# Performance work log

Measured on AMD Instinct MI355X. Metric: run time of the kernel, lower is better.

The kernel has to match this reference:

```python
import jax, jax.numpy as jnp
import numpy as np

ALPHA = 0.7
BETA = 0.3
GAMMA = 4.0
SMALL_LESION_WEIGHT = 10.0
SMOOTH = 1e-05
AREA_THRESH = 100  # region.area < 100 -> small lesion


def _label_components(mask):
    """8-connectivity connected-component labeling via min-label flooding.
    mask: [B,H,W] bool. Returns int32 labels in [0, H*W) for foreground,
    H*W (sentinel) for background. Equivalent partitioning to skimage.measure.label."""
    B, H, W = mask.shape
    BIG = H * W
    ids = jnp.arange(BIG, dtype=jnp.int32).reshape(1, H, W)
    lab0 = jnp.where(mask, ids, BIG)

    def neighbor_min(lab):
        p = jnp.pad(lab, ((0, 0), (1, 1), (1, 1)), constant_values=BIG)
        m = lab
        for di in range(3):  # 3x3 window = self + 8-neighbors
            for dj in range(3):
                m = jnp.minimum(m, p[:, di:di + H, dj:dj + W])
        return jnp.where(mask, m, BIG)

    def cond(state):
        return state[1]

    def body(state):
        lab, _ = state
        new = neighbor_min(lab)
        return new, jnp.any(new != lab)

    lab, _ = jax.lax.while_loop(cond, body, (lab0, jnp.array(True)))
    return lab


def _small_lesion_weights(targets):
    """targets: [B,1,H,W] float. Returns [B,1,H,W] weights: small_lesion_weight on
    pixels of connected components with area < AREA_THRESH, else 1.0."""
    t = targets[:, 0]                      # [B,H,W]
    mask = t > 0.5
    B, H, W = mask.shape
    BIG = H * W
    lab = _label_components(mask)          # [B,H,W] int32
    flat_lab = lab.reshape(B, BIG)
    ones = mask.astype(jnp.float32).reshape(B, BIG)
    # per-image component areas; background pixels fall into segment BIG
    areas = jax.vmap(lambda l, o: jax.ops.segment_sum(o, l, num_segments=BIG + 1))(flat_lab, ones)
    pix_area = jnp.take_along_axis(areas, flat_lab, axis=1).reshape(B, H, W)
    small = mask & (pix_area < AREA_THRESH)
    w = jnp.where(small, SMALL_LESION_WEIGHT, 1.0)
    return w[:, None, :, :]


def _bce_with_logits(x, t):
    # numerically stable elementwise BCE-with-logits
    return jnp.maximum(x, 0.0) - x * t + jnp.log1p(jnp.exp(-jnp.abs(x)))


def setup_inputs() -> dict:
    key = jax.random.key(0)
    k1, k2 = jax.random.split(key)
    B, C, H, W = 8, 1, 1024, 1024
    predictions = jax.random.normal(k1, (B, C, H, W), dtype=jnp.float32)
    targets = (jax.random.uniform(k2, (B, C, H, W)) < 0.05).astype(jnp.float32)
    return {"predictions": predictions, "targets": targets}


def reference(predictions, targets):
    p = jax.nn.sigmoid(predictions)

    # dice loss (global)
    inter = jnp.sum(p * targets)
    union = jnp.sum(p) + jnp.sum(targets)
    dice_loss = 1.0 - (2.0 * inter + SMOOTH) / (union + SMOOTH)

    # focal loss from logits
    bce = _bce_with_logits(predictions, targets)
    is_pos = targets == 1
    p_t = jnp.where(is_pos, p, 1.0 - p)
    alpha_t = jnp.where(is_pos, ALPHA, 1.0 - ALPHA)
    focal_loss = jnp.mean(alpha_t * (1.0 - p_t) ** GAMMA * bce)

    # tversky loss (FN-focused)
    TP = inter
    FP = jnp.sum((1.0 - targets) * p)
    FN = jnp.sum(targets * (1.0 - p))
    tversky_loss = 1.0 - (TP + SMOOTH) / (TP + ALPHA * FP + BETA * FN + SMOOTH)

    # small-lesion weighted BCE (weights are a non-diff function of targets)
    w = _small_lesion_weights(jax.lax.stop_gradient(targets))
    small_lesion_loss = jnp.mean(w * bce)

    return (dice_loss + focal_loss + tversky_loss + small_lesion_loss) / 4.0
```

## Files before the change

kernel.cpp:

```cpp
#include <hip/hip_runtime.h>

static constexpr int Bb = 8, Hh = 1024, Ww = 1024;
static constexpr int HW     = Hh * Ww;
static constexpr int NPIX   = Bb * HW;
static constexpr int NWORDS = NPIX / 64;
static constexpr int WPR    = Ww / 64;
static constexpr int WPI    = HW / 64;
static constexpr int NBK = 2048, NT = 256;
static constexpr int FNT = 1024;
static constexpr int FBG = 256;

typedef unsigned int u32;
typedef unsigned long long u64;

__device__ inline u32 lab_load(u32* L, u32 i) {
    return __hip_atomic_load(&L[i], __ATOMIC_RELAXED, __HIP_MEMORY_SCOPE_AGENT);
}
__device__ inline void lab_store(u32* L, u32 i, u32 v) {
    __hip_atomic_store(&L[i], v, __ATOMIC_RELAXED, __HIP_MEMORY_SCOPE_AGENT);
}
__device__ inline u32 find_root(u32* L, u32 x) {
    while (true) {
        u32 p = lab_load(L, x);
        if (p >= (u32)NPIX || p == x) return x;
        x = p;
    }
}
__device__ inline void union_labels(u32* L, u32 a, u32 b) {
    while (true) {
        a = find_root(L, a);
        b = find_root(L, b);
        if (a == b) return;
        if (a < b) { u32 t = a; a = b; b = t; }
        u32 old = atomicMin(&L[a], b);
        if (old == a || old >= (u32)NPIX) return;
        a = old;
    }
}

static constexpr u32 POISON = 0xAAAAAAAAu;
static constexpr u32 FLAGVAL = 0xC0FFEE00u;

__device__ inline double block_reduce(double v, double* lds) {
    for (int o = 32; o > 0; o >>= 1) v += __shfl_down(v, o, 64);
    int wave = threadIdx.x >> 6, lane = threadIdx.x & 63;
    __syncthreads();
    if (lane == 0) lds[wave] = v;
    __syncthreads();
    double r = 0.0;
    if (threadIdx.x == 0)
        for (int w = 0; w < (int)(blockDim.x >> 6); ++w) r += lds[w];
    return r;
}

__device__ inline float bce_pos(float x) {
    return fmaxf(-x, 0.0f) + __logf(1.0f + __expf(-fabsf(x)));
}

__device__ inline u64 spread4(u64 x) {
    x &= 0xFFFFull;
    x = (x | (x << 24)) & 0x000000FF000000FFull;
    x = (x | (x << 12)) & 0x000F000F000F000Full;
    x = (x | (x << 6))  & 0x0303030303030303ull;
    x = (x | (x << 3))  & 0x1111111111111111ull;
    return x;
}

__device__ inline void grid_barrier(u32* ctr, u32* flag) {
    __syncthreads();
    if (threadIdx.x == 0) {
        u32 old = __hip_atomic_fetch_add(ctr, 1u, __ATOMIC_RELAXED,
                                         __HIP_MEMORY_SCOPE_AGENT);
        if (old == POISON + (u32)FBG - 1u) {
            __hip_atomic_store(flag, FLAGVAL, __ATOMIC_RELAXED,
                               __HIP_MEMORY_SCOPE_AGENT);
        } else {
            while (__hip_atomic_load(flag, __ATOMIC_RELAXED,
                                     __HIP_MEMORY_SCOPE_AGENT) == POISON)
                __builtin_amdgcn_s_sleep(8);
        }
    }
    __syncthreads();
}

__global__ __launch_bounds__(NT) void k_init(const float4* __restrict__ pred4,
                                             const float4* __restrict__ targ4,
                                             u64* __restrict__ mask,
                                             double* __restrict__ part) {
    __shared__ double lds[NT / 64];
    float s_p = 0.f, s_t = 0.f, s_pt = 0.f, s_f = 0.f, s_b = 0.f, s_bf = 0.f;
    const int lane = threadIdx.x & 63;
    const int wid  = (blockIdx.x * NT + threadIdx.x) >> 6;

    float4 pv[4], tv[4];
    #pragma unroll
    for (int c = 0; c < 4; ++c) {
        const int chunk = (wid << 2) + c;
        pv[c] = pred4[chunk * 64 + lane];
        tv[c] = targ4[chunk * 64 + lane];
    }
    #pragma unroll
    for (int c = 0; c < 4; ++c) {
        const int chunk = (wid << 2) + c;
        const float* xa = &pv[c].x;
        const float* ta = &tv[c].x;
        u32 nib = 0;
        #pragma unroll
        for (int b = 0; b < 4; ++b) {
            const float x = xa[b], t = ta[b];
            const float ee  = __expf(-fabsf(x));
            const float rin = __builtin_amdgcn_rcpf(1.0f + ee);
            const float p   = (x >= 0.0f) ? rin : 1.0f - rin;
            const float bce = fmaxf(x, 0.0f) - x * t + __logf(1.0f + ee);
            const bool  pos = t > 0.5f;
            const float q1  = pos ? (1.0f - p) : p;
            const float at  = pos ? 0.7f : 0.3f;
            const float q2  = q1 * q1;
            s_p  += p;
            s_t  += t;
            s_pt += pos ? p : 0.0f;
            s_f  += at * q2 * q2 * bce;
            s_b  += bce;
            s_bf += pos ? bce : 0.0f;
            if (pos) nib |= 1u << b;
        }
        const u64 B0 = __ballot(nib & 1u);
        const u64 B1 = __ballot(nib & 2u);
        const u64 B2 = __ballot(nib & 4u);
        const u64 B3 = __ballot(nib & 8u);
        const int k = lane & 3;
        const u64 W = spread4(B0 >> (16 * k)) | (spread4(B1 >> (16 * k)) << 1)
                    | (spread4(B2 >> (16 * k)) << 2) | (spread4(B3 >> (16 * k)) << 3);
        if (lane < 4) mask[(chunk << 2) + lane] = W;
    }
    double r;
    r = block_reduce((double)s_p,  lds); if (threadIdx.x == 0) part[0 * NBK + blockIdx.x] = r;
    r = block_reduce((double)s_t,  lds); if (threadIdx.x == 0) part[1 * NBK + blockIdx.x] = r;
    r = block_reduce((double)s_pt, lds); if (threadIdx.x == 0) part[2 * NBK + blockIdx.x] = r;
    r = block_reduce((double)s_f,  lds); if (threadIdx.x == 0) part[3 * NBK + blockIdx.x] = r;
    r = block_reduce((double)s_b,  lds); if (threadIdx.x == 0) part[4 * NBK + blockIdx.x] = r;
    r = block_reduce((double)s_bf, lds); if (threadIdx.x == 0) part[5 * NBK + blockIdx.x] = r;
}

struct Nbr { u64 L, R, U, UL, UR, D, DL, DR; };
__device__ inline Nbr neighbors(const u64* __restrict__ mask, int wi, u64 cur) {
    int y  = (wi & (WPI - 1)) >> 4;
    int wx = wi & (WPR - 1);
    u64 lf = wx > 0       ? mask[wi - 1] : 0;
    u64 rt = wx < WPR - 1 ? mask[wi + 1] : 0;
    u64 up = 0, ul = 0, ur = 0, dn = 0, dl = 0, dr = 0;
    if (y > 0) {
        up = mask[wi - WPR];
        ul = wx > 0       ? mask[wi - WPR - 1] : 0;
        ur = wx < WPR - 1 ? mask[wi - WPR + 1] : 0;
    }
    if (y < Hh - 1) {
        dn = mask[wi + WPR];
        dl = wx > 0       ? mask[wi + WPR - 1] : 0;
        dr = wx < WPR - 1 ? mask[wi + WPR + 1] : 0;
    }
    Nbr n;
    n.L  = (cur << 1) | (lf >> 63);
    n.R  = (cur >> 1) | (rt << 63);
    n.U  = up;
    n.UL = (up << 1) | (ul >> 63);
    n.UR = (up >> 1) | (ur << 63);
    n.D  = dn;
    n.DL = (dn << 1) | (dl >> 63);
    n.DR = (dn >> 1) | (dr << 63);
    return n;
}

__device__ inline u64 half_mask(int t) {
    return (t & 1) ? 0xFFFFFFFF00000000ull : 0x00000000FFFFFFFFull;
}

static constexpr int B_CTR1 = 0, B_FLAG1 = 32, B_CTR2 = 64, B_FLAG2 = 96, B_DONE = 128;

__global__ __launch_bounds__(FNT, 4) void k_fused(const u64* __restrict__ mask,
                                                  u32* __restrict__ lab,
                                                  u32* __restrict__ area,
                                                  const float* __restrict__ pred,
                                                  double* __restrict__ part,
                                                  u32* __restrict__ bar,
                                                  float* __restrict__ out) {
    __shared__ double lds[FNT / 64];
    __shared__ int lastFlag;
    double* part_large = part + 6 * NBK;

    const int t  = blockIdx.x * FNT + threadIdx.x;
    const int wi = t >> 1;
    const u64 hm = half_mask(t);
    const u64 cur = mask[wi];
    const int base = wi << 6;

    u64 nonIso = 0, mrg = 0;
    u64 nL = 0, nU = 0, nUL = 0, nUR = 0;
    if (cur & hm) {
        Nbr n = neighbors(mask, wi, cur);
        nonIso = cur & (n.L | n.R | n.U | n.UL | n.UR | n.D | n.DL | n.DR) & hm;
        nL = n.L; nU = n.U; nUL = n.UL; nUR = n.UR;
        mrg = cur & (nL | nU | nUL | nUR) & hm;
    }

    u64 work = mrg;
    while (work) {
        int b = __builtin_ctzll(work); work &= work - 1;
        const u64 bit = 1ull << b;
        const u32 i = base + b;
        if (nL & bit) union_labels(lab, i, i - 1);
        if (nU & bit) union_labels(lab, i, i - Ww);
        else {
            if (nUL & bit) union_labels(lab, i, i - Ww - 1);
            if (nUR & bit) union_labels(lab, i, i - Ww + 1);
        }
    }
    grid_barrier(bar + B_CTR1, bar + B_FLAG1);

    u64 a = nonIso;
    while (a) {
        int b = __builtin_ctzll(a); a &= a - 1;
        const u32 i = base + b;
        const u32 r = find_root(lab, i);
        lab_store(lab, i, r);
        atomicAdd(&area[r], 1u);
    }
    grid_barrier(bar + B_CTR2, bar + B_FLAG2);

    float s = 0.f;
    u64 g = nonIso;
    while (g) {
        int b = __builtin_ctzll(g); g &= g - 1;
        const u32 i = base + b;
        const u32 r = lab_load(lab, i);
        const u32 cnt = __hip_atomic_load(&area[r], __ATOMIC_RELAXED,
                                          __HIP_MEMORY_SCOPE_AGENT) - POISON;
        if (cnt >= 100u)
            s += bce_pos(pred[i]);
    }
    double rr = block_reduce((double)s, lds);
    if (threadIdx.x == 0) {
        __hip_atomic_store(&part_large[blockIdx.x], rr, __ATOMIC_RELAXED,
                           __HIP_MEMORY_SCOPE_AGENT);
        asm volatile("s_waitcnt vmcnt(0)" ::: "memory");
        u32 old = __hip_atomic_fetch_add(bar + B_DONE, 1u, __ATOMIC_RELAXED,
                                         __HIP_MEMORY_SCOPE_AGENT);
        lastFlag = (old == POISON + (u32)FBG - 1u);
    }
    __syncthreads();
    if (!lastFlag) return;

    double sv[7] = {0, 0, 0, 0, 0, 0, 0};
    for (int j = threadIdx.x; j < NBK; j += FNT)
        #pragma unroll
        for (int k = 0; k < 6; ++k) sv[k] += part[k * NBK + j];
    for (int j = threadIdx.x; j < FBG; j += FNT)
        sv[6] += __hip_atomic_load(&part_large[j], __ATOMIC_RELAXED,
                                   __HIP_MEMORY_SCOPE_AGENT);
    double red[7];
    #pragma unroll
    for (int k = 0; k < 7; ++k) red[k] = block_reduce(sv[k], lds);
    if (threadIdx.x == 0) {
        double sum_p = red[0], sum_t = red[1], inter = red[2];
        double sum_f = red[3], sum_b = red[4], sum_bf = red[5], large_b = red[6];
        double small_b = sum_bf - large_b;
        double N = (double)NPIX;
        double dice    = 1.0 - (2.0 * inter + 1e-5) / (sum_p + sum_t + 1e-5);
        double focal   = sum_f / N;
        double FP = sum_p - inter, FN = sum_t - inter;
        double tversky = 1.0 - (inter + 1e-5) / (inter + 0.7 * FP + 0.3 * FN + 1e-5);
        double small   = (sum_b + 9.0 * small_b) / N;
        out[0] = (float)((dice + focal + tversky + small) * 0.25);
    }
}

extern "C" void kernel_launch(void* const* d_in, const int* in_sizes, int n_in,
                              void* d_out, int out_size, void* d_ws, size_t ws_size,
                              hipStream_t stream) {
    const float* pred = (const float*)d_in[0];
    const float* targ = (const float*)d_in[1];
    float* out = (float*)d_out;

    char* ws = (char*)d_ws;
    double* part = (double*)ws;
    u64* mask = (u64*)(ws + (size_t)(6 * NBK + FBG) * sizeof(double));
    u32* lab  = (u32*)(mask + NWORDS);
    u32* area = lab + NPIX;
    u32* bar  = area + NPIX;

    k_init <<<NBK, NT, 0, stream>>>((const float4*)pred, (const float4*)targ, mask, part);
    k_fused<<<FBG, FNT, 0, stream>>>(mask, lab, area, pred, part, bar, out);
}
```

Measured before the change: 151.3 us.

## Compact non-isolated foreground pixels into shared worklist for balanced union-find phases

Each block gathers its non-isolated foreground pixels, with packed neighbor flags, into a shared-memory worklist. The union, root-compression/area and weighted-BCE phases then iterate over that list with all threads striding through it, instead of each thread looping serially over its own bitmask. This targets warp divergence and load imbalance, since a few threads own many pixels while most own none. It costs 16KB of LDS per block, which may reduce occupancy with 1024-thread blocks, plus extra __syncthreads and an LDS atomic. An overflow path covers blocks with more than 4096 entries.

```diff
diff --git a/kernel.cpp b/kernel.cpp
--- a/kernel.cpp
+++ b/kernel.cpp
@@ -9,6 +9,7 @@
 static constexpr int NBK = 2048, NT = 256;
 static constexpr int FNT = 1024;
 static constexpr int FBG = 256;
+static constexpr int CAP = 4096;
 
 typedef unsigned int u32;
 typedef unsigned long long u64;
@@ -186,6 +187,8 @@
                                                   float* __restrict__ out) {
     __shared__ double lds[FNT / 64];
     __shared__ int lastFlag;
+    __shared__ u32 wl[CAP];
+    __shared__ u32 wl_n;
     double* part_large = part + 6 * NBK;
 
     const int t  = blockIdx.x * FNT + threadIdx.x;
@@ -194,49 +197,103 @@
     const u64 cur = mask[wi];
     const int base = wi << 6;
 
-    u64 nonIso = 0, mrg = 0;
+    if (threadIdx.x == 0) wl_n = 0;
+
+    u64 nonIso = 0;
     u64 nL = 0, nU = 0, nUL = 0, nUR = 0;
     if (cur & hm) {
         Nbr n = neighbors(mask, wi, cur);
         nonIso = cur & (n.L | n.R | n.U | n.UL | n.UR | n.D | n.DL | n.DR) & hm;
         nL = n.L; nU = n.U; nUL = n.UL; nUR = n.UR;
-        mrg = cur & (nL | nU | nUL | nUR) & hm;
-    }
-
-    u64 work = mrg;
-    while (work) {
-        int b = __builtin_ctzll(work); work &= work - 1;
-        const u64 bit = 1ull << b;
-        const u32 i = base + b;
-        if (nL & bit) union_labels(lab, i, i - 1);
-        if (nU & bit) union_labels(lab, i, i - Ww);
+    }
+    __syncthreads();
+
+    u64 ovf = 0;
+    {
+        int cnt = __builtin_popcountll(nonIso);
+        if (cnt) {
+            u32 slot = atomicAdd(&wl_n, (u32)cnt);
+            u64 w = nonIso;
+            while (w) {
+                int b = __builtin_ctzll(w); w &= w - 1;
+                if (slot < (u32)CAP) {
+                    const u32 f = (u32)((nL >> b) & 1) | ((u32)((nU >> b) & 1) << 1)
+                                | ((u32)((nUL >> b) & 1) << 2)
+                                | ((u32)((nUR >> b) & 1) << 3);
+                    wl[slot] = ((u32)(base + b) << 4) | f;
+                } else {
+                    ovf |= 1ull << b;
+                }
+                ++slot;
+            }
+        }
+    }
+    __syncthreads();
+    const u32 nwl = wl_n < (u32)CAP ? wl_n : (u32)CAP;
+
+    for (u32 e = threadIdx.x; e < nwl; e += FNT) {
+        const u32 ent = wl[e];
+        const u32 i = ent >> 4, f = ent & 15u;
+        if (f & 1u) union_labels(lab, i, i - 1);
+        if (f & 2u) union_labels(lab, i, i - Ww);
         else {
-            if (nUL & bit) union_labels(lab, i, i - Ww - 1);
-            if (nUR & bit) union_labels(lab, i, i - Ww + 1);
+            if (f & 4u) union_labels(lab, i, i - Ww - 1);
+            if (f & 8u) union_labels(lab, i, i - Ww + 1);
+        }
+    }
+    {
+        u64 w = ovf;
+        while (w) {
+            int b = __builtin_ctzll(w); w &= w - 1;
+            const u64 bit = 1ull << b;
+            const u32 i = base + b;
+            if (nL & bit) union_labels(lab, i, i - 1);
+            if (nU & bit) union_labels(lab, i, i - Ww);
+            else {
+                if (nUL & bit) union_labels(lab, i, i - Ww - 1);
+                if (nUR & bit) union_labels(lab, i, i - Ww + 1);
+            }
         }
     }
     grid_barrier(bar + B_CTR1, bar + B_FLAG1);
 
-    u64 a = nonIso;
-    while (a) {
-        int b = __builtin_ctzll(a); a &= a - 1;
-        const u32 i = base + b;
+    for (u32 e = threadIdx.x; e < nwl; e += FNT) {
+        const u32 i = wl[e] >> 4;
         const u32 r = find_root(lab, i);
         lab_store(lab, i, r);
         atomicAdd(&area[r], 1u);
     }
+    {
+        u64 w = ovf;
+        while (w) {
+            int b = __builtin_ctzll(w); w &= w - 1;
+            const u32 i = base + b;
+            const u32 r = find_root(lab, i);
+            lab_store(lab, i, r);
+            atomicAdd(&area[r], 1u);
+        }
+    }
     grid_barrier(bar + B_CTR2, bar + B_FLAG2);
 
     float s = 0.f;
-    u64 g = nonIso;
-    while (g) {
-        int b = __builtin_ctzll(g); g &= g - 1;
-        const u32 i = base + b;
+    for (u32 e = threadIdx.x; e < nwl; e += FNT) {
+        const u32 i = wl[e] >> 4;
         const u32 r = lab_load(lab, i);
         const u32 cnt = __hip_atomic_load(&area[r], __ATOMIC_RELAXED,
                                           __HIP_MEMORY_SCOPE_AGENT) - POISON;
         if (cnt >= 100u)
             s += bce_pos(pred[i]);
+    }
+    {
+        u64 w = ovf;
+        while (w) {
+            int b = __builtin_ctzll(w); w &= w - 1;
+            const u32 i = base + b;
+            const u32 r = lab_load(lab, i);
+            const u32 cnt = __hip_atomic_load(&area[r], __ATOMIC_RELAXED,
+                                              __HIP_MEMORY_SCOPE_AGENT) - POISON;
+            if (cnt >= 100u) s += bce_pos(pred[i]);
+        }
     }
     double rr = block_reduce((double)s, lds);
     if (threadIdx.x == 0) {
```

After: 140.4 us. -7.2%, faster.

## Do per-strip union-find in LDS and merge only strip-boundary components globally

Applied to the files above, without the earlier changes.

Each block now owns a 16-row strip and labels its components with union-find in shared memory. Per-root areas are packed into the LDS label word together with flag bits for a large component and for one that crosses the strip boundary. Only components touching a strip boundary go through global union-find and global area atomics, which cuts global atomic traffic and pointer chasing. The grid changes to 512 blocks of 512 threads with 64KB of dynamic LDS. The bit-packing adds complexity and limits each strip to 16K pixels and component sizes below 32K.

```diff
diff --git a/kernel.cpp b/kernel.cpp
--- a/kernel.cpp
+++ b/kernel.cpp
@@ -1,4 +1,7 @@
 #include <hip/hip_runtime.h>
+
+typedef unsigned int u32;
+typedef unsigned long long u64;
 
 static constexpr int Bb = 8, Hh = 1024, Ww = 1024;
 static constexpr int HW     = Hh * Ww;
@@ -7,11 +10,15 @@
 static constexpr int WPR    = Ww / 64;
 static constexpr int WPI    = HW / 64;
 static constexpr int NBK = 2048, NT = 256;
-static constexpr int FNT = 1024;
-static constexpr int FBG = 256;
-
-typedef unsigned int u32;
-typedef unsigned long long u64;
+static constexpr int FNT = 512, FBG = 512;
+static constexpr int SWORDS = NWORDS / FBG;
+static constexpr int SPX    = SWORDS * 64;
+
+static constexpr u32 POISON  = 0xAAAAAAAAu;
+static constexpr u32 FLAGVAL = 0xC0FFEE00u;
+static constexpr u32 LBITS = 0x3FFFu;
+static constexpr u32 BIGF  = 1u << 29;
+static constexpr u32 CROSSF = 1u << 30;
 
 __device__ inline u32 lab_load(u32* L, u32 i) {
     return __hip_atomic_load(&L[i], __ATOMIC_RELAXED, __HIP_MEMORY_SCOPE_AGENT);
@@ -38,8 +45,26 @@
     }
 }
 
-static constexpr u32 POISON = 0xAAAAAAAAu;
-static constexpr u32 FLAGVAL = 0xC0FFEE00u;
+__device__ inline u32 lds_load(u32* L, u32 x) {
+    return __hip_atomic_load(&L[x], __ATOMIC_RELAXED, __HIP_MEMORY_SCOPE_WORKGROUP);
+}
+__device__ inline void lds_store(u32* L, u32 x, u32 v) {
+    __hip_atomic_store(&L[x], v, __ATOMIC_RELAXED, __HIP_MEMORY_SCOPE_WORKGROUP);
+}
+__device__ inline u32 lfind(u32* L, u32 x) {
+    while (true) { u32 p = lds_load(L, x); if (p == x) return x; x = p; }
+}
+__device__ inline void lunion(u32* L, u32 a, u32 b) {
+    while (true) {
+        a = lfind(L, a);
+        b = lfind(L, b);
+        if (a == b) return;
+        if (a < b) { u32 t = a; a = b; b = t; }
+        u32 old = atomicMin(&L[a], b);
+        if (old == a) return;
+        a = old;
+    }
+}
 
 __device__ inline double block_reduce(double v, double* lds) {
     for (int o = 32; o > 0; o >>= 1) v += __shfl_down(v, o, 64);
@@ -184,83 +209,197 @@
                                                   double* __restrict__ part,
                                                   u32* __restrict__ bar,
                                                   float* __restrict__ out) {
-    __shared__ double lds[FNT / 64];
-    __shared__ int lastFlag;
+    extern __shared__ u32 llab[];
     double* part_large = part + 6 * NBK;
 
-    const int t  = blockIdx.x * FNT + threadIdx.x;
-    const int wi = t >> 1;
-    const u64 hm = half_mask(t);
-    const u64 cur = mask[wi];
-    const int base = wi << 6;
-
-    u64 nonIso = 0, mrg = 0;
-    u64 nL = 0, nU = 0, nUL = 0, nUR = 0;
+    const int tid  = threadIdx.x;
+    const int sbw  = blockIdx.x * SWORDS;
+    const int spx  = blockIdx.x * SPX;
+    const int lwi  = tid >> 1;
+    const int wi   = sbw + lwi;
+    const u64 hm   = half_mask(tid);
+    const u64 cur  = mask[wi];
+    const int lbase = lwi << 6;
+    const int y    = (wi & (WPI - 1)) >> 4;
+    const int ris  = y & 15;
+
+    u64 nL = 0, nU = 0, nUL = 0, nUR = 0, nUany = 0, nDany = 0;
     if (cur & hm) {
         Nbr n = neighbors(mask, wi, cur);
-        nonIso = cur & (n.L | n.R | n.U | n.UL | n.UR | n.D | n.DL | n.DR) & hm;
         nL = n.L; nU = n.U; nUL = n.UL; nUR = n.UR;
-        mrg = cur & (nL | nU | nUL | nUR) & hm;
-    }
-
-    u64 work = mrg;
-    while (work) {
-        int b = __builtin_ctzll(work); work &= work - 1;
-        const u64 bit = 1ull << b;
-        const u32 i = base + b;
-        if (nL & bit) union_labels(lab, i, i - 1);
-        if (nU & bit) union_labels(lab, i, i - Ww);
-        else {
-            if (nUL & bit) union_labels(lab, i, i - Ww - 1);
-            if (nUR & bit) union_labels(lab, i, i - Ww + 1);
+        nUany = n.U | n.UL | n.UR;
+        nDany = n.D | n.DL | n.DR;
+    }
+
+    for (u32 j = tid; j < (u32)SPX; j += FNT) llab[j] = j;
+    __syncthreads();
+
+    {
+        const u64 uU  = ris > 0 ? nU  : 0;
+        const u64 uUL = ris > 0 ? nUL : 0;
+        const u64 uUR = ris > 0 ? nUR : 0;
+        u64 w = cur & (nL | uU | uUL | uUR) & hm;
+        while (w) {
+            int b = __builtin_ctzll(w); w &= w - 1;
+            const u64 bit = 1ull << b;
+            const u32 li = lbase + b;
+            if (nL & bit) lunion(llab, li, li - 1);
+            if (uU & bit) lunion(llab, li, li - 1024);
+            else {
+                if (uUL & bit) lunion(llab, li, li - 1025);
+                if (uUR & bit) lunion(llab, li, li - 1023);
+            }
+        }
+    }
+    __syncthreads();
+
+    {
+        u64 w = cur & hm;
+        while (w) {
+            int b = __builtin_ctzll(w); w &= w - 1;
+            const u32 li = lbase + b;
+            const u32 r = lfind(llab, li);
+            if (r != li) lds_store(llab, li, r);
+        }
+    }
+    __syncthreads();
+
+    {
+        u64 w = cur & hm;
+        while (w) {
+            int b = __builtin_ctzll(w); w &= w - 1;
+            const u32 li = lbase + b;
+            const u32 r = lds_load(llab, li) & LBITS;
+            atomicAdd(&llab[r], 1u << 14);
+        }
+    }
+    __syncthreads();
+
+    if (cur & hm) {
+        if (ris == 0) {
+            u64 w = cur & nUany & hm;
+            while (w) {
+                int b = __builtin_ctzll(w); w &= w - 1;
+                const u32 r = lds_load(llab, lbase + b) & LBITS;
+                atomicOr(&llab[r], CROSSF);
+            }
+        }
+        if (ris == 15) {
+            u64 w = cur & nDany & hm;
+            while (w) {
+                int b = __builtin_ctzll(w); w &= w - 1;
+                const u32 r = lds_load(llab, lbase + b) & LBITS;
+                atomicOr(&llab[r], CROSSF);
+            }
+        }
+    }
+    __syncthreads();
+
+    {
+        u64 w = cur & hm;
+        while (w) {
+            int b = __builtin_ctzll(w); w &= w - 1;
+            const u32 li = lbase + b;
+            const u32 e = lds_load(llab, li);
+            if ((e & LBITS) == li && !(e & CROSSF)) {
+                const u32 cnt = (e >> 14) & 0x7FFFu;
+                if (cnt >= 100u) lds_store(llab, li, e | BIGF);
+            }
+        }
+    }
+    if (ris == 0 && (cur & hm)) {
+        u64 w = cur & nUany & hm;
+        while (w) {
+            int b = __builtin_ctzll(w); w &= w - 1;
+            const u64 bit = 1ull << b;
+            const u32 li = lbase + b;
+            const u32 gi = spx + li;
+            const u32 gr = spx + (lds_load(llab, li) & LBITS);
+            if (nU  & bit) union_labels(lab, gr, gi - Ww);
+            if (nUL & bit) union_labels(lab, gr, gi - Ww - 1);
+            if (nUR & bit) union_labels(lab, gr, gi - Ww + 1);
+        }
+    }
+    if (ris == 15 && (cur & hm)) {
+        u64 w = cur & nDany & hm;
+        while (w) {
+            int b = __builtin_ctzll(w); w &= w - 1;
+            const u32 li = lbase + b;
+            union_labels(lab, spx + li, spx + (lds_load(llab, li) & LBITS));
         }
     }
     grid_barrier(bar + B_CTR1, bar + B_FLAG1);
 
-    u64 a = nonIso;
-    while (a) {
-        int b = __builtin_ctzll(a); a &= a - 1;
-        const u32 i = base + b;
-        const u32 r = find_root(lab, i);
-        lab_store(lab, i, r);
-        atomicAdd(&area[r], 1u);
+    {
+        u64 w = cur & hm;
+        while (w) {
+            int b = __builtin_ctzll(w); w &= w - 1;
+            const u32 li = lbase + b;
+            const u32 e = lds_load(llab, li);
+            if ((e & LBITS) == li && (e & CROSSF)) {
+                const u32 gr = find_root(lab, spx + li);
+                lab_store(lab, spx + li, gr);
+                atomicAdd(&area[gr], (e >> 14) & 0x7FFFu);
+            }
+        }
     }
     grid_barrier(bar + B_CTR2, bar + B_FLAG2);
 
+    {
+        u64 w = cur & hm;
+        while (w) {
+            int b = __builtin_ctzll(w); w &= w - 1;
+            const u32 li = lbase + b;
+            const u32 e = lds_load(llab, li);
+            if ((e & LBITS) == li && (e & CROSSF)) {
+                const u32 gr  = lab_load(lab, spx + li);
+                const u32 tot = __hip_atomic_load(&area[gr], __ATOMIC_RELAXED,
+                                                  __HIP_MEMORY_SCOPE_AGENT) - POISON;
+                if (tot >= 100u) lds_store(llab, li, e | BIGF);
+            }
+        }
+    }
+    __syncthreads();
+
     float s = 0.f;
-    u64 g = nonIso;
-    while (g) {
-        int b = __builtin_ctzll(g); g &= g - 1;
-        const u32 i = base + b;
-        const u32 r = lab_load(lab, i);
-        const u32 cnt = __hip_atomic_load(&area[r], __ATOMIC_RELAXED,
-                                          __HIP_MEMORY_SCOPE_AGENT) - POISON;
-        if (cnt >= 100u)
-            s += bce_pos(pred[i]);
-    }
-    double rr = block_reduce((double)s, lds);
-    if (threadIdx.x == 0) {
+    {
+        u64 w = cur & hm;
+        while (w) {
+            int b = __builtin_ctzll(w); w &= w - 1;
+            const u32 li = lbase + b;
+            const u32 e = lds_load(llab, li);
+            const u32 r = e & LBITS;
+            const u32 f = (r == li) ? e : lds_load(llab, r);
+            if (f & BIGF) s += bce_pos(pred[spx + li]);
+        }
+    }
+    __syncthreads();
+    double* rlds   = (double*)llab;
+    int* lastFlagP = (int*)&llab[32];
+
+    double rr = block_reduce((double)s, rlds);
+    if (tid == 0) {
         __hip_atomic_store(&part_large[blockIdx.x], rr, __ATOMIC_RELAXED,
                            __HIP_MEMORY_SCOPE_AGENT);
         asm volatile("s_waitcnt vmcnt(0)" ::: "memory");
         u32 old = __hip_atomic_fetch_add(bar + B_DONE, 1u, __ATOMIC_RELAXED,
                                          __HIP_MEMORY_SCOPE_AGENT);
-        lastFlag = (old == POISON + (u32)FBG - 1u);
-    }
-    __syncthreads();
-    if (!lastFlag) return;
+        *lastFlagP = (old == POISON + (u32)FBG - 1u);
+    }
+    __syncthreads();
+    if (!*lastFlagP) return;
 
     double sv[7] = {0, 0, 0, 0, 0, 0, 0};
-    for (int j = threadIdx.x; j < NBK; j += FNT)
+    for (int j = tid; j < NBK; j += FNT)
         #pragma unroll
         for (int k = 0; k < 6; ++k) sv[k] += part[k * NBK + j];
-    for (int j = threadIdx.x; j < FBG; j += FNT)
+    for (int j = tid; j < FBG; j += FNT)
         sv[6] += __hip_atomic_load(&part_large[j], __ATOMIC_RELAXED,
                                    __HIP_MEMORY_SCOPE_AGENT);
     double red[7];
     #pragma unroll
-    for (int k = 0; k < 7; ++k) red[k] = block_reduce(sv[k], lds);
-    if (threadIdx.x == 0) {
+    for (int k = 0; k < 7; ++k) red[k] = block_reduce(sv[k], rlds);
+    if (tid == 0) {
         double sum_p = red[0], sum_t = red[1], inter = red[2];
         double sum_f = red[3], sum_b = red[4], sum_bf = red[5], large_b = red[6];
         double small_b = sum_bf - large_b;
@@ -289,5 +428,6 @@
     u32* bar  = area + NPIX;
 
     k_init <<<NBK, NT, 0, stream>>>((const float4*)pred, (const float4*)targ, mask, part);
-    k_fused<<<FBG, FNT, 0, stream>>>(mask, lab, area, pred, part, bar, out);
-}
+    k_fused<<<FBG, FNT, (size_t)SPX * sizeof(u32), stream>>>(mask, lab, area, pred,
+                                                             part, bar, out);
+}
```

Result: faster. 144.2 us (-4.7%).
